# Performance work log

Measured on AMD Instinct MI355X. Metric: run time of the kernel, lower is better.

## Reference

```python
import math
import jax, jax.numpy as jnp
import numpy as np

S, D = 4096, 1024          # cur_seq, input_dim
H, Dh = 8, 64              # head_num, head_dim
ETA, R = 4, 8              # eta, r
E = Dh * ETA               # feature-mapped key dim = eta*head_dim = 256
EPS = 1e-5


def setup_inputs() -> dict:
    key = jax.random.key(0)
    ks = jax.random.split(key, 8)
    inputs = jax.random.normal(ks[0], (S, D), jnp.float32) * 0.1
    terminations = (jax.random.uniform(ks[1], (S,)) < 0.01).astype(jnp.int32)
    W_kqv = jax.random.normal(ks[2], (D, H * Dh * 5), jnp.float32) / np.sqrt(D).astype(np.float32)
    b_kqv = jnp.zeros((H * Dh * 5,), jnp.float32)
    W_p = jax.random.normal(ks[3], (D, H * ETA * 3), jnp.float32) / np.sqrt(D).astype(np.float32)
    b_p = jnp.zeros((H * ETA * 3,), jnp.float32)
    W_proj = jax.random.normal(ks[4], (H * Dh, D), jnp.float32) / np.sqrt(H * Dh).astype(np.float32)
    b_proj = jnp.zeros((D,), jnp.float32)
    tilde_k_prev = jnp.zeros((R, H, E), jnp.float32)
    tilde_v_prev = jnp.zeros((R, H, Dh), jnp.float32)
    s_prev = jnp.zeros((H, E), jnp.float32)
    tick = jnp.ones((1,), jnp.float32)
    return dict(inputs=inputs, terminations=terminations, W_kqv=W_kqv, b_kqv=b_kqv,
                W_p=W_p, b_p=b_p, W_proj=W_proj, b_proj=b_proj,
                tilde_k_prev=tilde_k_prev, tilde_v_prev=tilde_v_prev,
                s_prev=s_prev, tick=tick)


def reference(inputs, terminations, W_kqv, b_kqv, W_p, b_p, W_proj, b_proj,
              tilde_k_prev, tilde_v_prev, s_prev, tick):
    # fused projections
    kqvbg = (inputs @ W_kqv + b_kqv).reshape(S, H, 5, Dh)
    k, q, v, beta, g = (kqvbg[:, :, i] for i in range(5))
    p = (inputs @ W_p + b_p).reshape(S, H, 3, ETA)
    p1, p2, p3 = p[:, :, 0], p[:, :, 1], p[:, :, 2]

    # feature maps: outer product over (Dh, ETA), flattened with Dh outer (matches torch flatten(-2))
    keys = (jax.nn.relu(k)[..., :, None] * jax.nn.relu(p1)[..., None, :]).reshape(S, H, E)
    queries = (jax.nn.relu(q)[..., :, None] * jax.nn.relu(p2)[..., None, :]).reshape(S, H, E)
    gammas = (jax.nn.sigmoid(g)[..., :, None] * jax.nn.sigmoid(p3)[..., None, :]).reshape(S, H, E)
    beta = jax.nn.sigmoid(beta)  # (S,H,Dh)

    # oscillation basis
    ticks = tick[0] + jnp.arange(1, S + 1, dtype=inputs.dtype)       # (S,)
    omegas = jnp.linspace(-math.pi, math.pi, R).astype(inputs.dtype)  # (R,)
    occil = jnp.cos(ticks[:, None] * omegas[None, :])                 # (S,R)

    vals = v * beta                                                   # (S,H,Dh)
    vals_r = vals[:, None] * occil[:, :, None, None]                  # (S,R,H,Dh)
    keys_g = keys * gammas                                            # (S,H,E)
    s_seq = keys_g
    keys_r = keys_g[:, None] * occil[:, :, None, None]                # (S,R,H,E)

    nt = (1.0 - terminations.astype(inputs.dtype))[:, None, None]
    dg = (1.0 - gammas) * nt                                          # (S,H,E)
    db = (1.0 - beta) * nt                                            # (S,H,Dh)

    def step(carry, xs):
        kc, vc, sc = carry
        kt, vt, st, dgt, dbt = xs
        kc = dgt[None] * kc + kt   # (R,H,E)
        vc = dbt[None] * vc + vt   # (R,H,Dh)
        sc = dgt * sc + st         # (H,E)
        return (kc, vc, sc), (kc, vc, sc)

    _, (fk, fv, fs) = jax.lax.scan(step, (tilde_k_prev, tilde_v_prev, s_prev),
                                   (keys_r, vals_r, s_seq, dg, db))

    kdq = jnp.einsum('srhe,she->srh', fk, queries)
    kv = jnp.einsum('srhd,srh->shd', fv, kdq)
    norm = jnp.einsum('she,she->sh', fs, queries)
    attn = kv / (2.0 * R * norm[..., None] + EPS)                     # (S,H,Dh)
    out = attn.reshape(S, H * Dh) @ W_proj + b_proj                   # (S,D)
    return out
```

## Files before the change

kernel.cpp:

```cpp
#include <hip/hip_runtime.h>
#include <hip/hip_bf16.h>

#define S_    4096
#define D_    1024
#define H_    8
#define DH_   64
#define ETA_  4
#define R_    8
#define E_    256
#define NC_   256
#define LC_   (S_/NC_)
#define N1_   2688
#define NKQV_ 2560
#define NP_   96
#define PIF   3.14159265358979323846

#define PB_CVT    2048
#define PB_TRWK   (PB_CVT + 640)
#define PB_TRWP   (PB_TRWK + 32)
#define PB_TRWPJ  (PB_TRWP + 128)
#define PB_OC     (PB_TRWPJ + 128)
#define PB_BIAS   (PB_OC + 11)
#define PB_TOTAL  PB_BIAS

typedef unsigned short u16;
typedef unsigned int   u32;
typedef _Float16 v8h __attribute__((ext_vector_type(8)));
typedef float v4f __attribute__((ext_vector_type(4)));

__device__ __forceinline__ u16 f2h(float f) {
    _Float16 h = (_Float16)f;
    return __builtin_bit_cast(unsigned short, h);
}
__device__ __forceinline__ float h2f(u16 u) {
    return (float)__builtin_bit_cast(_Float16, u);
}
__device__ __forceinline__ float sigm(float x) { return 1.f / (1.f + expf(-x)); }

#define GLD16(gp, lp) __builtin_amdgcn_global_load_lds( \
    (const __attribute__((address_space(1))) u32*)(const void*)(gp), \
    (__attribute__((address_space(3))) u32*)(void*)(lp), 16, 0, 0)


__device__ __forceinline__ void tr64h(float (*tile)[65], const float* __restrict__ src, int K, int Nsrc,
                                      u16* __restrict__ dH, int rowOff, int k0, int n0, int t) {
    const int cc = t & 63, rr = t >> 6;
    const int nkt = K >> 5;
    #pragma unroll
    for (int i = 0; i < 16; ++i) {
        int kk = rr * 16 + i;
        tile[kk][cc] = (n0 + cc < Nsrc) ? src[(size_t)(k0 + kk) * Nsrc + n0 + cc] : 0.f;
    }
    __syncthreads();
    #pragma unroll
    for (int i = 0; i < 16; ++i) {
        int nn = rr * 16 + i;
        int nrow = rowOff + n0 + nn, k = k0 + cc;
        int nt = nrow >> 4, kt = k >> 5;
        int ln = (nrow & 15) + (((k & 31) >> 3) << 4), j = k & 7;
        dH[((size_t)(nt * nkt + kt) << 9) + ln * 8 + j] = f2h(tile[cc][nn]);
    }
}

__global__ __launch_bounds__(256) void prep_all(const float* __restrict__ inputs,
                                                const float* __restrict__ Wk, const float* __restrict__ Wp,
                                                const float* __restrict__ Wproj,
                                                const float* __restrict__ bk, const float* __restrict__ bp,
                                                const float* __restrict__ tick,
                                                u16* __restrict__ AbfH, u16* __restrict__ AbfL,
                                                u16* __restrict__ BTh, u16* __restrict__ WpTh,
                                                float* __restrict__ biasb, float* __restrict__ OC) {
    __shared__ float tile[64][65];
    const int b = blockIdx.x, t = threadIdx.x;
    if (b < PB_CVT) {
        int i = b * 256 + t;
        const float4* xp = (const float4*)inputs;
        float4 a = xp[2 * i], bb = xp[2 * i + 1];
        float v[8] = {a.x, a.y, a.z, a.w, bb.x, bb.y, bb.z, bb.w};
        unsigned hh[8], ll[8];
        #pragma unroll
        for (int j = 0; j < 8; ++j) {
            u16 h = f2h(v[j]);
            hh[j] = h;
            ll[j] = f2h(v[j] - h2f(h));
        }
        uint4 rh, rl;
        rh.x = hh[0] | (hh[1] << 16); rh.y = hh[2] | (hh[3] << 16);
        rh.z = hh[4] | (hh[5] << 16); rh.w = hh[6] | (hh[7] << 16);
        rl.x = ll[0] | (ll[1] << 16); rl.y = ll[2] | (ll[3] << 16);
        rl.z = ll[4] | (ll[5] << 16); rl.w = ll[6] | (ll[7] << 16);
        ((uint4*)AbfH)[i] = rh;
        ((uint4*)AbfL)[i] = rl;
    } else if (b < PB_TRWK) {
        int i = b - PB_CVT;
        tr64h(tile, Wk, D_, NKQV_, BTh, 0, (i % 16) * 64, (i / 16) * 64, t);
    } else if (b < PB_TRWP) {
        int i = b - PB_TRWK;
        tr64h(tile, Wp, D_, NP_, BTh, NKQV_, (i % 16) * 64, (i / 16) * 64, t);
    } else if (b < PB_TRWPJ) {
        int i = b - PB_TRWP;
        tr64h(tile, Wproj, 512, D_, WpTh, 0, (i % 8) * 64, (i / 8) * 64, t);
    } else if (b < PB_OC) {
        int idx = (b - PB_TRWPJ) * 256 + t;
        int tt = idx / R_, r = idx % R_;
        float start = (float)(-PIF), stop = (float)PIF;
        float step = __fdiv_rn(__fsub_rn(stop, start), 7.0f);
        float om = __fadd_rn(start, __fmul_rn((float)r, step));
        float tk = __fadd_rn(tick[0], (float)(tt + 1));
        OC[idx] = cosf(__fmul_rn(tk, om));
    } else {
        int n = (b - PB_OC) * 256 + t;
        if (n < N1_)
            biasb[n] = n < NKQV_ ? bk[n] : (n < NKQV_ + NP_ ? bp[n - NKQV_] : 0.f);
    }
}

__global__ __launch_bounds__(256, 3) void gemm_x2_hyb(const u16* __restrict__ Ah, const u16* __restrict__ Al,
                                                      const u16* __restrict__ BTf,
                                                      const float* __restrict__ bias,
                                                      float* __restrict__ Yo, int ldy, int Kdim, int actMode) {
    __shared__ __align__(16) u16 lds[2][2][4096];
    const int tid = threadIdx.x, lane = tid & 63, w = tid >> 6;
    const int mw = (w >> 1) * 64, nw = (w & 1) * 64;
    const int l15 = lane & 15, lk8 = lane >> 4;
    const int lke = (lk8 ^ (l15 & 3) ^ ((l15 >> 2) & 3)) * 8;
    const int gx = gridDim.x;
    const int nb = gx * gridDim.y;
    const int orig = blockIdx.y * gx + blockIdx.x;
    const int per = nb >> 3;
    const int swz = (orig & 7) * per + (orig >> 3);
    const int m0 = (swz / gx) * 128, n0 = (swz % gx) * 128;
    const int nkt = Kdim >> 5;

    auto stageA = [&](int buf, int k0) {
        #pragma unroll
        for (int c = 0; c < 2; ++c) {
            int u = tid + (c << 8);
            int row = u >> 2, s = u & 3;
            int kc = ((s ^ (row & 3) ^ ((row >> 2) & 3)) << 3);
            int wub = ((u & ~63) << 3);
            size_t offA = (size_t)(m0 + row) * Kdim + k0 + kc;
            GLD16(Ah + offA, &lds[buf][0][wub]);
            GLD16(Al + offA, &lds[buf][1][wub]);
        }
    };

    size_t bBase[4];
    #pragma unroll
    for (int f = 0; f < 4; ++f)
        bBase[f] = ((size_t)(((n0 + nw) >> 4) + f) * nkt << 9) + lane * 8;

    v4f acc[4][4] = {};
    stageA(0, 0);
    v8h bcur[4];
    #pragma unroll
    for (int f = 0; f < 4; ++f) bcur[f] = *(const v8h*)(BTf + bBase[f]);
    int cur = 0;
    for (int kt = 0; kt < nkt; ++kt) {
        __syncthreads();
        if (kt + 1 < nkt) stageA(cur ^ 1, (kt + 1) << 5);
        v8h bnxt[4];
        if (kt + 1 < nkt) {
            const size_t ko = (size_t)(kt + 1) << 9;
            #pragma unroll
            for (int f = 0; f < 4; ++f) bnxt[f] = *(const v8h*)(BTf + bBase[f] + ko);
        }
        v8h afh[4], afl[4];
        #pragma unroll
        for (int f = 0; f < 4; ++f) {
            int ra = (mw + f * 16 + l15) * 32 + lke;
            afh[f] = *(const v8h*)&lds[cur][0][ra];
            afl[f] = *(const v8h*)&lds[cur][1][ra];
        }
        #pragma unroll
        for (int i = 0; i < 4; ++i)
            #pragma unroll
            for (int j = 0; j < 4; ++j)
                acc[i][j] = __builtin_amdgcn_mfma_f32_16x16x32_f16(afh[i], bcur[j], acc[i][j], 0, 0, 0);
        #pragma unroll
        for (int i = 0; i < 4; ++i)
            #pragma unroll
            for (int j = 0; j < 4; ++j)
                acc[i][j] = __builtin_amdgcn_mfma_f32_16x16x32_f16(afl[i], bcur[j], acc[i][j], 0, 0, 0);
        if (kt + 1 < nkt) {
            #pragma unroll
            for (int f = 0; f < 4; ++f) bcur[f] = bnxt[f];
        }
        cur ^= 1;
    }
    #pragma unroll
    for (int i = 0; i < 4; ++i) {
        int row0 = m0 + mw + i * 16 + lk8 * 4;
        #pragma unroll
        for (int j = 0; j < 4; ++j) {
            int col = n0 + nw + j * 16 + l15;
            float bv = bias[col];
            int ct = 2;
            if (actMode) {
                if (col < NKQV_) ct = (col % 320) >> 6;
                else { int m12 = (col - NKQV_) % 12; ct = (m12 < 8) ? 0 : 3; }
            }
            #pragma unroll
            for (int rg = 0; rg < 4; ++rg) {
                float y = acc[i][j][rg] + bv;
                if (ct == 0 || ct == 1) y = fmaxf(y, 0.f);
                else if (ct >= 3) y = sigm(y);
                Yo[(size_t)(row0 + rg) * ldy + col] = y;
            }
        }
    }
}

__global__ __launch_bounds__(64) void scan_p1(const float* __restrict__ Y1, const float* __restrict__ OC,
                                              const int* __restrict__ term, float* __restrict__ CL) {
    const int b = blockIdx.x, c = b / H_, h = b % H_, lane = threadIdx.x;
    float kc[R_][ETA_] = {}, vc[R_] = {}, sc[ETA_] = {};
    float Pg[ETA_] = {1.f, 1.f, 1.f, 1.f}, Pb = 1.f;
    for (int t = c * LC_; t < c * LC_ + LC_; ++t) {
        const float* row = Y1 + (size_t)t * N1_;
        const float* bh = row + h * 320;
        float rk = bh[lane], vv = bh[128 + lane], sb = bh[192 + lane], sg = bh[256 + lane];
        const float* pp = row + NKQV_ + h * 12;
        float nt = 1.f - (float)term[t];
        float vals = vv * sb, dbv = (1.f - sb) * nt;
        float occ[R_];
        #pragma unroll
        for (int r = 0; r < R_; ++r) occ[r] = OC[t * R_ + r];
        #pragma unroll
        for (int e = 0; e < ETA_; ++e) {
            float gam = sg * pp[8 + e];
            float kg = rk * pp[e] * gam;
            float dgv = (1.f - gam) * nt;
            sc[e] = dgv * sc[e] + kg;
            Pg[e] *= dgv;
            #pragma unroll
            for (int r = 0; r < R_; ++r) kc[r][e] = dgv * kc[r][e] + kg * occ[r];
        }
        Pb *= dbv;
        #pragma unroll
        for (int r = 0; r < R_; ++r) vc[r] = dbv * vc[r] + vals * occ[r];
    }
    float* out = CL + (size_t)b * 49 * 64;
    #pragma unroll
    for (int r = 0; r < R_; ++r)
        #pragma unroll
        for (int e = 0; e < ETA_; ++e) out[(r * 4 + e) * 64 + lane] = kc[r][e];
    #pragma unroll
    for (int r = 0; r < R_; ++r) out[(32 + r) * 64 + lane] = vc[r];
    #pragma unroll
    for (int e = 0; e < ETA_; ++e) out[(40 + e) * 64 + lane] = sc[e];
    #pragma unroll
    for (int e = 0; e < ETA_; ++e) out[(44 + e) * 64 + lane] = Pg[e];
    out[48 * 64 + lane] = Pb;
}

__global__ __launch_bounds__(64) void scan_comb(const float* __restrict__ CL, float* __restrict__ CI,
                                                const float* __restrict__ TK, const float* __restrict__ TV,
                                                const float* __restrict__ SP) {
    const int gid = blockIdx.x * 64 + threadIdx.x;
    const int lane = gid & 63;
    const int hv = gid >> 6;
    const int h = hv / 44;
    const int v = hv % 44;
    float x;
    int dvec;
    if (v < 32) {
        int r = v >> 2, e = v & 3;
        x = TK[((size_t)r * H_ + h) * E_ + lane * 4 + e];
        dvec = 44 + e;
    } else if (v < 40) {
        int r = v - 32;
        x = TV[((size_t)r * H_ + h) * DH_ + lane];
        dvec = 48;
    } else {
        int e = v - 40;
        x = SP[(size_t)h * E_ + lane * 4 + e];
        dvec = 44 + e;
    }
    const float* clb = CL + (size_t)h * 49 * 64 + (size_t)v * 64 + lane;
    const float* dcb = CL + (size_t)h * 49 * 64 + (size_t)dvec * 64 + lane;
    float* cib = CI + (size_t)h * 44 * 64 + (size_t)v * 64 + lane;
    const size_t sCL = (size_t)H_ * 49 * 64;
    const size_t sCI = (size_t)H_ * 44 * 64;
    #pragma unroll 8
    for (int c = 0; c < NC_; ++c) {
        cib[(size_t)c * sCI] = x;
        float cl = clb[(size_t)c * sCL];
        float d  = dcb[(size_t)c * sCL];
        x = fmaf(d, x, cl);
    }
}

__global__ __launch_bounds__(64) void scan_p3(const float* __restrict__ Y1, const float* __restrict__ OC,
                                              const int* __restrict__ term, const float* __restrict__ CI,
                                              u16* __restrict__ attnH, u16* __restrict__ attnL) {
    const int b = blockIdx.x, c = b / H_, h = b % H_, lane = threadIdx.x;
    float kc[R_][ETA_], vc[R_], sc[ETA_];
    const float* ci = CI + (size_t)b * 44 * 64;
    #pragma unroll
    for (int r = 0; r < R_; ++r)
        #pragma unroll
        for (int e = 0; e < ETA_; ++e) kc[r][e] = ci[(r * 4 + e) * 64 + lane];
    #pragma unroll
    for (int r = 0; r < R_; ++r) vc[r] = ci[(32 + r) * 64 + lane];
    #pragma unroll
    for (int e = 0; e < ETA_; ++e) sc[e] = ci[(40 + e) * 64 + lane];
    for (int t = c * LC_; t < c * LC_ + LC_; ++t) {
        const float* row = Y1 + (size_t)t * N1_;
        const float* bh = row + h * 320;
        float rk = bh[lane], rq = bh[64 + lane], vv = bh[128 + lane], sb = bh[192 + lane], sg = bh[256 + lane];
        const float* pp = row + NKQV_ + h * 12;
        float nt = 1.f - (float)term[t];
        float vals = vv * sb, dbv = (1.f - sb) * nt;
        float occ[R_];
        #pragma unroll
        for (int r = 0; r < R_; ++r) occ[r] = OC[t * R_ + r];
        float qe[ETA_];
        #pragma unroll
        for (int e = 0; e < ETA_; ++e) {
            float gam = sg * pp[8 + e];
            float kg = rk * pp[e] * gam;
            float dgv = (1.f - gam) * nt;
            qe[e] = rq * pp[4 + e];
            sc[e] = dgv * sc[e] + kg;
            #pragma unroll
            for (int r = 0; r < R_; ++r) kc[r][e] = dgv * kc[r][e] + kg * occ[r];
        }
        #pragma unroll
        for (int r = 0; r < R_; ++r) vc[r] = dbv * vc[r] + vals * occ[r];
        float kdq[R_], nrm = 0.f;
        #pragma unroll
        for (int r = 0; r < R_; ++r) {
            float s = 0.f;
            #pragma unroll
            for (int e = 0; e < ETA_; ++e) s += kc[r][e] * qe[e];
            kdq[r] = s;
        }
        #pragma unroll
        for (int e = 0; e < ETA_; ++e) nrm += sc[e] * qe[e];
        #pragma unroll
        for (int m = 1; m < 64; m <<= 1) {
            #pragma unroll
            for (int r = 0; r < R_; ++r) kdq[r] += __shfl_xor(kdq[r], m);
            nrm += __shfl_xor(nrm, m);
        }
        float kv = 0.f;
        #pragma unroll
        for (int r = 0; r < R_; ++r) kv += vc[r] * kdq[r];
        float at = kv / (2.f * R_ * nrm + 1e-5f);
        size_t oi = (size_t)t * (H_ * DH_) + h * DH_ + lane;
        u16 hi = f2h(at);
        attnH[oi] = hi;
        attnL[oi] = f2h(at - h2f(hi));
    }
}

extern "C" void kernel_launch(void* const* d_in, const int* in_sizes, int n_in,
                              void* d_out, int out_size, void* d_ws, size_t ws_size,
                              hipStream_t stream) {
    const float* inputs = (const float*)d_in[0];
    const int*   term   = (const int*)d_in[1];
    const float* Wk     = (const float*)d_in[2];
    const float* bk     = (const float*)d_in[3];
    const float* Wp     = (const float*)d_in[4];
    const float* bp     = (const float*)d_in[5];
    const float* Wproj  = (const float*)d_in[6];
    const float* bproj  = (const float*)d_in[7];
    const float* TK     = (const float*)d_in[8];
    const float* TV     = (const float*)d_in[9];
    const float* SP     = (const float*)d_in[10];
    const float* tick   = (const float*)d_in[11];
    float* out = (float*)d_out;

    char* w = (char*)d_ws;
    u16* AbfH   = (u16*)w;  w += (size_t)S_ * D_ * 2;
    u16* AbfL   = (u16*)w;  w += (size_t)S_ * D_ * 2;
    u16* BTh    = (u16*)w;  w += (size_t)N1_ * D_ * 2;
    u16* WpTh   = (u16*)w;  w += (size_t)D_ * 512 * 2;
    u16* attnH  = (u16*)w;  w += (size_t)S_ * 512 * 2;
    u16* attnL  = (u16*)w;  w += (size_t)S_ * 512 * 2;
    float* biasb = (float*)w; w += (size_t)N1_ * 4;
    float* Y1   = (float*)w; w += (size_t)S_ * N1_ * 4;
    float* OC   = (float*)w; w += (size_t)S_ * R_ * 4;
    float* CL   = (float*)w; w += (size_t)NC_ * H_ * 49 * 64 * 4;
    float* CI   = (float*)w; w += (size_t)NC_ * H_ * 44 * 64 * 4;

    prep_all<<<PB_TOTAL, 256, 0, stream>>>(inputs, Wk, Wp, Wproj, bk, bp, tick,
                                           AbfH, AbfL, BTh, WpTh, biasb, OC);
    gemm_x2_hyb<<<dim3(N1_ / 128, S_ / 128), 256, 0, stream>>>(AbfH, AbfL, BTh, biasb, Y1, N1_, D_, 1);
    scan_p1<<<NC_ * H_, 64, 0, stream>>>(Y1, OC, term, CL);
    scan_comb<<<(H_ * 44 * 64) / 64, 64, 0, stream>>>(CL, CI, TK, TV, SP);
    scan_p3<<<NC_ * H_, 64, 0, stream>>>(Y1, OC, term, CI, attnH, attnL);
    gemm_x2_hyb<<<dim3(1024 / 128, S_ / 128), 256, 0, stream>>>(attnH, attnL, WpTh, bproj, out, D_, 512, 0);
}
```

Baseline: 161.6 us.

## Fuse three scan phases into one cooperative kernel with grid syncs

Merges the chunk-local scan, the cross-chunk combine and the final scan/output pass into a single cooperative kernel separated by grid-wide barriers. This removes two kernel launches and their inter-kernel gaps. In exchange it requires all 2048 64-thread blocks to be co-resident (launch bounds hint of 2 per SIMD), and the grid syncs add barrier cost; the combine phase still runs on only 352 blocks while the rest wait.

New measurement: 611.5 us. 278% more time.

```diff
diff --git a/kernel.cpp b/kernel.cpp
--- a/kernel.cpp
+++ b/kernel.cpp
@@ -1,5 +1,8 @@
 #include <hip/hip_runtime.h>
 #include <hip/hip_bf16.h>
+#include <hip/hip_cooperative_groups.h>
+
+namespace cg = cooperative_groups;
 
 #define S_    4096
 #define D_    1024
@@ -211,147 +214,151 @@
     }
 }
 
-__global__ __launch_bounds__(64) void scan_p1(const float* __restrict__ Y1, const float* __restrict__ OC,
-                                              const int* __restrict__ term, float* __restrict__ CL) {
+__global__ __launch_bounds__(64, 2) void scan_fused(const float* __restrict__ Y1, const float* __restrict__ OC,
+                                                    const int* __restrict__ term,
+                                                    const float* __restrict__ TK, const float* __restrict__ TV,
+                                                    const float* __restrict__ SP,
+                                                    float* __restrict__ CL, float* __restrict__ CI,
+                                                    u16* __restrict__ attnH, u16* __restrict__ attnL) {
+    cg::grid_group grid = cg::this_grid();
     const int b = blockIdx.x, c = b / H_, h = b % H_, lane = threadIdx.x;
-    float kc[R_][ETA_] = {}, vc[R_] = {}, sc[ETA_] = {};
-    float Pg[ETA_] = {1.f, 1.f, 1.f, 1.f}, Pb = 1.f;
-    for (int t = c * LC_; t < c * LC_ + LC_; ++t) {
-        const float* row = Y1 + (size_t)t * N1_;
-        const float* bh = row + h * 320;
-        float rk = bh[lane], vv = bh[128 + lane], sb = bh[192 + lane], sg = bh[256 + lane];
-        const float* pp = row + NKQV_ + h * 12;
-        float nt = 1.f - (float)term[t];
-        float vals = vv * sb, dbv = (1.f - sb) * nt;
-        float occ[R_];
-        #pragma unroll
-        for (int r = 0; r < R_; ++r) occ[r] = OC[t * R_ + r];
-        #pragma unroll
-        for (int e = 0; e < ETA_; ++e) {
-            float gam = sg * pp[8 + e];
-            float kg = rk * pp[e] * gam;
-            float dgv = (1.f - gam) * nt;
-            sc[e] = dgv * sc[e] + kg;
-            Pg[e] *= dgv;
-            #pragma unroll
-            for (int r = 0; r < R_; ++r) kc[r][e] = dgv * kc[r][e] + kg * occ[r];
-        }
-        Pb *= dbv;
-        #pragma unroll
-        for (int r = 0; r < R_; ++r) vc[r] = dbv * vc[r] + vals * occ[r];
-    }
-    float* out = CL + (size_t)b * 49 * 64;
-    #pragma unroll
-    for (int r = 0; r < R_; ++r)
-        #pragma unroll
-        for (int e = 0; e < ETA_; ++e) out[(r * 4 + e) * 64 + lane] = kc[r][e];
-    #pragma unroll
-    for (int r = 0; r < R_; ++r) out[(32 + r) * 64 + lane] = vc[r];
-    #pragma unroll
-    for (int e = 0; e < ETA_; ++e) out[(40 + e) * 64 + lane] = sc[e];
-    #pragma unroll
-    for (int e = 0; e < ETA_; ++e) out[(44 + e) * 64 + lane] = Pg[e];
-    out[48 * 64 + lane] = Pb;
-}
-
-__global__ __launch_bounds__(64) void scan_comb(const float* __restrict__ CL, float* __restrict__ CI,
-                                                const float* __restrict__ TK, const float* __restrict__ TV,
-                                                const float* __restrict__ SP) {
-    const int gid = blockIdx.x * 64 + threadIdx.x;
-    const int lane = gid & 63;
-    const int hv = gid >> 6;
-    const int h = hv / 44;
-    const int v = hv % 44;
-    float x;
-    int dvec;
-    if (v < 32) {
-        int r = v >> 2, e = v & 3;
-        x = TK[((size_t)r * H_ + h) * E_ + lane * 4 + e];
-        dvec = 44 + e;
-    } else if (v < 40) {
-        int r = v - 32;
-        x = TV[((size_t)r * H_ + h) * DH_ + lane];
-        dvec = 48;
-    } else {
-        int e = v - 40;
-        x = SP[(size_t)h * E_ + lane * 4 + e];
-        dvec = 44 + e;
-    }
-    const float* clb = CL + (size_t)h * 49 * 64 + (size_t)v * 64 + lane;
-    const float* dcb = CL + (size_t)h * 49 * 64 + (size_t)dvec * 64 + lane;
-    float* cib = CI + (size_t)h * 44 * 64 + (size_t)v * 64 + lane;
-    const size_t sCL = (size_t)H_ * 49 * 64;
-    const size_t sCI = (size_t)H_ * 44 * 64;
-    #pragma unroll 8
-    for (int c = 0; c < NC_; ++c) {
-        cib[(size_t)c * sCI] = x;
-        float cl = clb[(size_t)c * sCL];
-        float d  = dcb[(size_t)c * sCL];
-        x = fmaf(d, x, cl);
-    }
-}
-
-__global__ __launch_bounds__(64) void scan_p3(const float* __restrict__ Y1, const float* __restrict__ OC,
-                                              const int* __restrict__ term, const float* __restrict__ CI,
-                                              u16* __restrict__ attnH, u16* __restrict__ attnL) {
-    const int b = blockIdx.x, c = b / H_, h = b % H_, lane = threadIdx.x;
-    float kc[R_][ETA_], vc[R_], sc[ETA_];
-    const float* ci = CI + (size_t)b * 44 * 64;
-    #pragma unroll
-    for (int r = 0; r < R_; ++r)
-        #pragma unroll
-        for (int e = 0; e < ETA_; ++e) kc[r][e] = ci[(r * 4 + e) * 64 + lane];
-    #pragma unroll
-    for (int r = 0; r < R_; ++r) vc[r] = ci[(32 + r) * 64 + lane];
-    #pragma unroll
-    for (int e = 0; e < ETA_; ++e) sc[e] = ci[(40 + e) * 64 + lane];
-    for (int t = c * LC_; t < c * LC_ + LC_; ++t) {
-        const float* row = Y1 + (size_t)t * N1_;
-        const float* bh = row + h * 320;
-        float rk = bh[lane], rq = bh[64 + lane], vv = bh[128 + lane], sb = bh[192 + lane], sg = bh[256 + lane];
-        const float* pp = row + NKQV_ + h * 12;
-        float nt = 1.f - (float)term[t];
-        float vals = vv * sb, dbv = (1.f - sb) * nt;
-        float occ[R_];
-        #pragma unroll
-        for (int r = 0; r < R_; ++r) occ[r] = OC[t * R_ + r];
-        float qe[ETA_];
-        #pragma unroll
-        for (int e = 0; e < ETA_; ++e) {
-            float gam = sg * pp[8 + e];
-            float kg = rk * pp[e] * gam;
-            float dgv = (1.f - gam) * nt;
-            qe[e] = rq * pp[4 + e];
-            sc[e] = dgv * sc[e] + kg;
-            #pragma unroll
-            for (int r = 0; r < R_; ++r) kc[r][e] = dgv * kc[r][e] + kg * occ[r];
-        }
-        #pragma unroll
-        for (int r = 0; r < R_; ++r) vc[r] = dbv * vc[r] + vals * occ[r];
-        float kdq[R_], nrm = 0.f;
-        #pragma unroll
-        for (int r = 0; r < R_; ++r) {
-            float s = 0.f;
-            #pragma unroll
-            for (int e = 0; e < ETA_; ++e) s += kc[r][e] * qe[e];
-            kdq[r] = s;
-        }
-        #pragma unroll
-        for (int e = 0; e < ETA_; ++e) nrm += sc[e] * qe[e];
-        #pragma unroll
-        for (int m = 1; m < 64; m <<= 1) {
-            #pragma unroll
-            for (int r = 0; r < R_; ++r) kdq[r] += __shfl_xor(kdq[r], m);
-            nrm += __shfl_xor(nrm, m);
-        }
-        float kv = 0.f;
-        #pragma unroll
-        for (int r = 0; r < R_; ++r) kv += vc[r] * kdq[r];
-        float at = kv / (2.f * R_ * nrm + 1e-5f);
-        size_t oi = (size_t)t * (H_ * DH_) + h * DH_ + lane;
-        u16 hi = f2h(at);
-        attnH[oi] = hi;
-        attnL[oi] = f2h(at - h2f(hi));
+
+    {
+        float kc[R_][ETA_] = {}, vc[R_] = {}, sc[ETA_] = {};
+        float Pg[ETA_] = {1.f, 1.f, 1.f, 1.f}, Pb = 1.f;
+        for (int t = c * LC_; t < c * LC_ + LC_; ++t) {
+            const float* row = Y1 + (size_t)t * N1_;
+            const float* bh = row + h * 320;
+            float rk = bh[lane], vv = bh[128 + lane], sb = bh[192 + lane], sg = bh[256 + lane];
+            const float* pp = row + NKQV_ + h * 12;
+            float nt = 1.f - (float)term[t];
+            float vals = vv * sb, dbv = (1.f - sb) * nt;
+            float occ[R_];
+            #pragma unroll
+            for (int r = 0; r < R_; ++r) occ[r] = OC[t * R_ + r];
+            #pragma unroll
+            for (int e = 0; e < ETA_; ++e) {
+                float gam = sg * pp[8 + e];
+                float kg = rk * pp[e] * gam;
+                float dgv = (1.f - gam) * nt;
+                sc[e] = dgv * sc[e] + kg;
+                Pg[e] *= dgv;
+                #pragma unroll
+                for (int r = 0; r < R_; ++r) kc[r][e] = dgv * kc[r][e] + kg * occ[r];
+            }
+            Pb *= dbv;
+            #pragma unroll
+            for (int r = 0; r < R_; ++r) vc[r] = dbv * vc[r] + vals * occ[r];
+        }
+        float* out = CL + (size_t)b * 49 * 64;
+        #pragma unroll
+        for (int r = 0; r < R_; ++r)
+            #pragma unroll
+            for (int e = 0; e < ETA_; ++e) out[(r * 4 + e) * 64 + lane] = kc[r][e];
+        #pragma unroll
+        for (int r = 0; r < R_; ++r) out[(32 + r) * 64 + lane] = vc[r];
+        #pragma unroll
+        for (int e = 0; e < ETA_; ++e) out[(40 + e) * 64 + lane] = sc[e];
+        #pragma unroll
+        for (int e = 0; e < ETA_; ++e) out[(44 + e) * 64 + lane] = Pg[e];
+        out[48 * 64 + lane] = Pb;
+    }
+    grid.sync();
+
+    if (b < (H_ * 44 * 64) / 64) {
+        const int gid = b * 64 + lane;
+        const int hv = gid >> 6;
+        const int hh = hv / 44;
+        const int v = hv % 44;
+        float x;
+        int dvec;
+        if (v < 32) {
+            int r = v >> 2, e = v & 3;
+            x = TK[((size_t)r * H_ + hh) * E_ + (gid & 63) * 4 + e];
+            dvec = 44 + e;
+        } else if (v < 40) {
+            int r = v - 32;
+            x = TV[((size_t)r * H_ + hh) * DH_ + (gid & 63)];
+            dvec = 48;
+        } else {
+            int e = v - 40;
+            x = SP[(size_t)hh * E_ + (gid & 63) * 4 + e];
+            dvec = 44 + e;
+        }
+        const float* clb = CL + (size_t)hh * 49 * 64 + (size_t)v * 64 + (gid & 63);
+        const float* dcb = CL + (size_t)hh * 49 * 64 + (size_t)dvec * 64 + (gid & 63);
+        float* cib = CI + (size_t)hh * 44 * 64 + (size_t)v * 64 + (gid & 63);
+        const size_t sCL = (size_t)H_ * 49 * 64;
+        const size_t sCI = (size_t)H_ * 44 * 64;
+        #pragma unroll 8
+        for (int cc = 0; cc < NC_; ++cc) {
+            cib[(size_t)cc * sCI] = x;
+            float cl = clb[(size_t)cc * sCL];
+            float d  = dcb[(size_t)cc * sCL];
+            x = fmaf(d, x, cl);
+        }
+    }
+    grid.sync();
+
+    {
+        float kc[R_][ETA_], vc[R_], sc[ETA_];
+        const float* ci = CI + (size_t)b * 44 * 64;
+        #pragma unroll
+        for (int r = 0; r < R_; ++r)
+            #pragma unroll
+            for (int e = 0; e < ETA_; ++e) kc[r][e] = ci[(r * 4 + e) * 64 + lane];
+        #pragma unroll
+        for (int r = 0; r < R_; ++r) vc[r] = ci[(32 + r) * 64 + lane];
+        #pragma unroll
+        for (int e = 0; e < ETA_; ++e) sc[e] = ci[(40 + e) * 64 + lane];
+        for (int t = c * LC_; t < c * LC_ + LC_; ++t) {
+            const float* row = Y1 + (size_t)t * N1_;
+            const float* bh = row + h * 320;
+            float rk = bh[lane], rq = bh[64 + lane], vv = bh[128 + lane], sb = bh[192 + lane], sg = bh[256 + lane];
+            const float* pp = row + NKQV_ + h * 12;
+            float nt = 1.f - (float)term[t];
+            float vals = vv * sb, dbv = (1.f - sb) * nt;
+            float occ[R_];
+            #pragma unroll
+            for (int r = 0; r < R_; ++r) occ[r] = OC[t * R_ + r];
+            float qe[ETA_];
+            #pragma unroll
+            for (int e = 0; e < ETA_; ++e) {
+                float gam = sg * pp[8 + e];
+                float kg = rk * pp[e] * gam;
+                float dgv = (1.f - gam) * nt;
+                qe[e] = rq * pp[4 + e];
+                sc[e] = dgv * sc[e] + kg;
+                #pragma unroll
+                for (int r = 0; r < R_; ++r) kc[r][e] = dgv * kc[r][e] + kg * occ[r];
+            }
+            #pragma unroll
+            for (int r = 0; r < R_; ++r) vc[r] = dbv * vc[r] + vals * occ[r];
+            float kdq[R_], nrm = 0.f;
+            #pragma unroll
+            for (int r = 0; r < R_; ++r) {
+                float s = 0.f;
+                #pragma unroll
+                for (int e = 0; e < ETA_; ++e) s += kc[r][e] * qe[e];
+                kdq[r] = s;
+            }
+            #pragma unroll
+            for (int e = 0; e < ETA_; ++e) nrm += sc[e] * qe[e];
+            #pragma unroll
+            for (int m = 1; m < 64; m <<= 1) {
+                #pragma unroll
+                for (int r = 0; r < R_; ++r) kdq[r] += __shfl_xor(kdq[r], m);
+                nrm += __shfl_xor(nrm, m);
+            }
+            float kv = 0.f;
+            #pragma unroll
+            for (int r = 0; r < R_; ++r) kv += vc[r] * kdq[r];
+            float at = kv / (2.f * R_ * nrm + 1e-5f);
+            size_t oi = (size_t)t * (H_ * DH_) + h * DH_ + lane;
+            u16 hi = f2h(at);
+            attnH[oi] = hi;
+            attnL[oi] = f2h(at - h2f(hi));
+        }
     }
 }
 
@@ -388,8 +395,10 @@
     prep_all<<<PB_TOTAL, 256, 0, stream>>>(inputs, Wk, Wp, Wproj, bk, bp, tick,
                                            AbfH, AbfL, BTh, WpTh, biasb, OC);
     gemm_x2_hyb<<<dim3(N1_ / 128, S_ / 128), 256, 0, stream>>>(AbfH, AbfL, BTh, biasb, Y1, N1_, D_, 1);
-    scan_p1<<<NC_ * H_, 64, 0, stream>>>(Y1, OC, term, CL);
-    scan_comb<<<(H_ * 44 * 64) / 64, 64, 0, stream>>>(CL, CI, TK, TV, SP);
-    scan_p3<<<NC_ * H_, 64, 0, stream>>>(Y1, OC, term, CI, attnH, attnL);
+    {
+        void* args[] = {(void*)&Y1, (void*)&OC, (void*)&term, (void*)&TK, (void*)&TV, (void*)&SP,
+                        (void*)&CL, (void*)&CI, (void*)&attnH, (void*)&attnL};
+        hipLaunchCooperativeKernel((void*)scan_fused, dim3(NC_ * H_), dim3(64), args, 0, stream);
+    }
     gemm_x2_hyb<<<dim3(1024 / 128, S_ / 128), 256, 0, stream>>>(attnH, attnL, WpTh, bproj, out, D_, 512, 0);
 }
```

## Add 64-row-tile GEMM with register-streamed B for output projection

Applied to the files above, without the earlier changes.

Adds a specialized GEMM for the final projection. It uses 64x128 tiles instead of 128x128, which doubles the block count (512 blocks) so more of the GPU is occupied. A tiles are double-buffered in LDS through direct global-to-LDS loads, while B fragments come straight from a pre-laid-out weight buffer into registers and are prefetched one k-step ahead. Block indices are also swizzled, which may help L2 locality. The trade is less reuse per tile and more B traffic through registers.

New measurement: 156.4 us. 1.03x faster.

```diff
diff --git a/kernel.cpp b/kernel.cpp
--- a/kernel.cpp
+++ b/kernel.cpp
@@ -211,6 +211,89 @@
     }
 }
 
+__global__ __launch_bounds__(256, 6) void gemm_x2_g2(const u16* __restrict__ Ah, const u16* __restrict__ Al,
+                                                     const u16* __restrict__ BTf,
+                                                     const float* __restrict__ bias,
+                                                     float* __restrict__ Yo, int ldy, int Kdim) {
+    __shared__ __align__(16) u16 lds[2][2][2048];
+    const int tid = threadIdx.x, lane = tid & 63, w = tid >> 6;
+    const int nw = w * 32;
+    const int l15 = lane & 15, lk8 = lane >> 4;
+    const int lke = (lk8 ^ (l15 & 3) ^ ((l15 >> 2) & 3)) * 8;
+    const int gx = gridDim.x;
+    const int nb = gx * gridDim.y;
+    const int orig = blockIdx.y * gx + blockIdx.x;
+    const int per = nb >> 3;
+    const int swz = (orig & 7) * per + (orig >> 3);
+    const int m0 = (swz / gx) * 64, n0 = (swz % gx) * 128;
+    const int nkt = Kdim >> 5;
+
+    auto stageA = [&](int buf, int k0) {
+        int row = tid >> 2, s = tid & 3;
+        int kc = ((s ^ (row & 3) ^ ((row >> 2) & 3)) << 3);
+        int wub = ((tid & ~63) << 3);
+        size_t offA = (size_t)(m0 + row) * Kdim + k0 + kc;
+        GLD16(Ah + offA, &lds[buf][0][wub]);
+        GLD16(Al + offA, &lds[buf][1][wub]);
+    };
+
+    size_t bBase[2];
+    #pragma unroll
+    for (int f = 0; f < 2; ++f)
+        bBase[f] = ((size_t)(((n0 + nw) >> 4) + f) * nkt << 9) + lane * 8;
+
+    v4f acc[4][2] = {};
+    stageA(0, 0);
+    v8h bcur[2];
+    #pragma unroll
+    for (int f = 0; f < 2; ++f) bcur[f] = *(const v8h*)(BTf + bBase[f]);
+    int cur = 0;
+    for (int kt = 0; kt < nkt; ++kt) {
+        __syncthreads();
+        if (kt + 1 < nkt) stageA(cur ^ 1, (kt + 1) << 5);
+        v8h bnxt[2];
+        if (kt + 1 < nkt) {
+            const size_t ko = (size_t)(kt + 1) << 9;
+            #pragma unroll
+            for (int f = 0; f < 2; ++f) bnxt[f] = *(const v8h*)(BTf + bBase[f] + ko);
+        }
+        v8h afh[4], afl[4];
+        #pragma unroll
+        for (int f = 0; f < 4; ++f) {
+            int ra = (f * 16 + l15) * 32 + lke;
+            afh[f] = *(const v8h*)&lds[cur][0][ra];
+            afl[f] = *(const v8h*)&lds[cur][1][ra];
+        }
+        #pragma unroll
+        for (int i = 0; i < 4; ++i)
+            #pragma unroll
+            for (int j = 0; j < 2; ++j)
+                acc[i][j] = __builtin_amdgcn_mfma_f32_16x16x32_f16(afh[i], bcur[j], acc[i][j], 0, 0, 0);
+        #pragma unroll
+        for (int i = 0; i < 4; ++i)
+            #pragma unroll
+            for (int j = 0; j < 2; ++j)
+                acc[i][j] = __builtin_amdgcn_mfma_f32_16x16x32_f16(afl[i], bcur[j], acc[i][j], 0, 0, 0);
+        if (kt + 1 < nkt) {
+            #pragma unroll
+            for (int f = 0; f < 2; ++f) bcur[f] = bnxt[f];
+        }
+        cur ^= 1;
+    }
+    #pragma unroll
+    for (int i = 0; i < 4; ++i) {
+        int row0 = m0 + i * 16 + lk8 * 4;
+        #pragma unroll
+        for (int j = 0; j < 2; ++j) {
+            int col = n0 + nw + j * 16 + l15;
+            float bv = bias[col];
+            #pragma unroll
+            for (int rg = 0; rg < 4; ++rg)
+                Yo[(size_t)(row0 + rg) * ldy + col] = acc[i][j][rg] + bv;
+        }
+    }
+}
+
 __global__ __launch_bounds__(64) void scan_p1(const float* __restrict__ Y1, const float* __restrict__ OC,
                                               const int* __restrict__ term, float* __restrict__ CL) {
     const int b = blockIdx.x, c = b / H_, h = b % H_, lane = threadIdx.x;
@@ -391,5 +474,5 @@
     scan_p1<<<NC_ * H_, 64, 0, stream>>>(Y1, OC, term, CL);
     scan_comb<<<(H_ * 44 * 64) / 64, 64, 0, stream>>>(CL, CI, TK, TV, SP);
     scan_p3<<<NC_ * H_, 64, 0, stream>>>(Y1, OC, term, CI, attnH, attnL);
-    gemm_x2_hyb<<<dim3(1024 / 128, S_ / 128), 256, 0, stream>>>(attnH, attnL, WpTh, bproj, out, D_, 512, 0);
-}
+    gemm_x2_g2<<<dim3(1024 / 128, S_ / 64), 256, 0, stream>>>(attnH, attnL, WpTh, bproj, out, D_, 512);
+}
```
